# Optimization experiments

Hardware: AMD Instinct MI355X
Metric: run time of the kernel (lower is better)

## Reference

```python
import jax, jax.numpy as jnp
import numpy as np
import math


def _bilinear_sample(fea, gx, gy):
    # fea: (C, Hs, Ws); gx, gy: (P,) pixel coords. zeros padding, align_corners=True.
    C, Hs, Ws = fea.shape
    x0 = jnp.floor(gx)
    y0 = jnp.floor(gy)
    wx = gx - x0
    wy = gy - y0

    def tap(xi, yi):
        valid = (xi >= 0) & (xi <= Ws - 1) & (yi >= 0) & (yi <= Hs - 1)
        xc = jnp.clip(xi, 0, Ws - 1).astype(jnp.int32)
        yc = jnp.clip(yi, 0, Hs - 1).astype(jnp.int32)
        return fea[:, yc, xc] * valid.astype(fea.dtype)  # (C, P)

    return (tap(x0, y0) * (1 - wx) * (1 - wy)
            + tap(x0 + 1, y0) * wx * (1 - wy)
            + tap(x0, y0 + 1) * (1 - wx) * wy
            + tap(x0 + 1, y0 + 1) * wx * wy)


def homo_warping(src_fea, src_proj, ref_proj, depth_values):
    # src_fea: (B,C,Hs,Ws); projs: (B,4,4); depth_values: (B,D,Hr,Wr)
    B, C, Hs, Ws = src_fea.shape
    _, D, Hr, Wr = depth_values.shape
    proj = src_proj @ jnp.linalg.inv(ref_proj)
    rot = proj[:, :3, :3]
    trans = proj[:, :3, 3:4]
    yy, xx = jnp.meshgrid(jnp.arange(Hr, dtype=src_fea.dtype),
                          jnp.arange(Wr, dtype=src_fea.dtype), indexing='ij')
    xyz = jnp.stack([xx.ravel(), yy.ravel(), jnp.ones(Hr * Wr, src_fea.dtype)])  # (3, HW)
    rot_xyz = jnp.einsum('bij,jp->bip', rot, xyz)  # (B,3,HW)
    pts = rot_xyz[:, :, None, :] * depth_values.reshape(B, 1, D, Hr * Wr) + trans[:, :, :, None]
    z = pts[:, 2]
    z = jnp.where(z == 0, 1e-9, z)
    # grid is computed under torch.no_grad() in the original -> stop_gradient
    gx = jax.lax.stop_gradient((pts[:, 0] / z).reshape(B, D * Hr * Wr))
    gy = jax.lax.stop_gradient((pts[:, 1] / z).reshape(B, D * Hr * Wr))
    warped = jax.vmap(_bilinear_sample)(src_fea, gx, gy)  # (B, C, D*Hr*Wr)
    return warped.reshape(B, C, D, Hr, Wr)


def setup_inputs() -> dict:
    key = jax.random.key(0)
    B, C, H, W, D, N = 2, 32, 128, 160, 32, 4
    k1, k2, k3 = jax.random.split(key, 3)
    ref_feature = jax.random.normal(k1, (B, C, H, W), jnp.float32)
    src_features = jax.random.normal(k2, (N, B, C, H, W), jnp.float32)
    # proj_matrices: (B, nviews, 2, 4, 4); [...,0]=extrinsic 4x4, [...,1]=intrinsic 4x4
    K = np.eye(4, dtype=np.float32)
    K[0, 0] = 300.0; K[1, 1] = 300.0; K[0, 2] = W / 2.0; K[1, 2] = H / 2.0
    projs = np.zeros((B, N + 1, 2, 4, 4), np.float32)
    for v in range(N + 1):
        a = 0.03 * v
        Rm = np.array([[np.cos(a), 0.0, np.sin(a)],
                       [0.0, 1.0, 0.0],
                       [-np.sin(a), 0.0, np.cos(a)]], np.float32)
        E = np.eye(4, dtype=np.float32)
        E[:3, :3] = Rm
        E[:3, 3] = np.array([20.0 * v, 5.0 * v, 0.0], np.float32)
        projs[:, v, 0] = E
        projs[:, v, 1] = K
    proj_matrices = jnp.asarray(projs)
    depth_hypo = jnp.broadcast_to(
        jnp.linspace(425.0, 935.0, D, dtype=jnp.float32)[None, :, None, None], (B, D, H, W))
    reg_w = jax.random.normal(k3, (8,), jnp.float32)
    reg_b = jnp.zeros((1,), jnp.float32)
    return {"ref_feature": ref_feature, "src_features": src_features,
            "proj_matrices": proj_matrices, "depth_hypo": depth_hypo,
            "reg_w": reg_w, "reg_b": reg_b}


def reference(ref_feature, src_features, proj_matrices, depth_hypo, reg_w, reg_b):
    attn_temp = 2.0
    G = 8  # group_cor_dim; group_cor=True path
    B, D, H, W = depth_hypo.shape
    C = ref_feature.shape[1]
    ref_proj = proj_matrices[:, 0]
    ref_proj_new = ref_proj[:, 0].at[:, :3, :4].set(
        jnp.einsum('bij,bjk->bik', ref_proj[:, 1, :3, :3], ref_proj[:, 0, :3, :4]))
    # ref_volume broadcast over D via size-1 depth axis (B,G,C/G,1,H,W)
    ref_g = ref_feature.reshape(B, G, C // G, 1, H, W)
    cor_weight_sum = 1e-8
    cor_feats = 0.0
    n_src = src_features.shape[0]
    for src_idx in range(n_src):  # fixed small number of source views
        src_proj = proj_matrices[:, src_idx + 1]
        src_proj_new = src_proj[:, 0].at[:, :3, :4].set(
            jnp.einsum('bij,bjk->bik', src_proj[:, 1, :3, :3], src_proj[:, 0, :3, :4]))
        warped = homo_warping(src_features[src_idx], src_proj_new, ref_proj_new, depth_hypo)
        cor_feat = (warped.reshape(B, G, C // G, D, H, W) * ref_g).mean(2)  # (B,G,D,H,W)
        cor_weight = jax.nn.softmax(cor_feat.sum(1) / attn_temp, axis=1) / math.sqrt(C)  # (B,D,H,W)
        cor_weight_sum = cor_weight_sum + cor_weight
        cor_feats = cor_feats + cor_weight[:, None] * cor_feat
    cor_feats = cor_feats / cor_weight_sum[:, None]
    # regnet stand-in: 1x1x1 conv over the G group channels -> (B,D,H,W) logits
    attn_logits = jnp.einsum('bgdhw,g->bdhw', cor_feats, reg_w) + reg_b[0]
    attn_weight = jax.nn.softmax(attn_logits, axis=1)
    idx = jnp.argmax(attn_weight, axis=1, keepdims=True)
    depth = jnp.take_along_axis(depth_hypo, idx, axis=1).squeeze(1)  # (B,H,W)
    return depth, attn_weight
```

## Files before the change

kernel.cpp:

```cpp
#include <hip/hip_runtime.h>
#include <hip/hip_bf16.h>
#include <math.h>

#define BB 2
#define CC 32
#define HH 128
#define WW 160
#define DD 32
#define NN 4
#define HW (HH * WW)
#define GG 8

typedef float v2f __attribute__((ext_vector_type(2)));

__device__ void compute_mats(int t, const float* __restrict__ proj,
                             float* __restrict__ mats) {
    int b = t >> 2, n = t & 3;
    const float* Er = proj + ((size_t)(b * (NN + 1) + 0) * 2 + 0) * 16;
    const float* Kr = proj + ((size_t)(b * (NN + 1) + 0) * 2 + 1) * 16;
    const float* Es = proj + ((size_t)(b * (NN + 1) + n + 1) * 2 + 0) * 16;
    const float* Ks = proj + ((size_t)(b * (NN + 1) + n + 1) * 2 + 1) * 16;

    double A[4][4], Bm[4][4];
    for (int r = 0; r < 4; r++)
        for (int c = 0; c < 4; c++) {
            if (r < 3) {
                A[r][c]  = (double)Kr[r*4+0]*Er[0*4+c] + (double)Kr[r*4+1]*Er[1*4+c] + (double)Kr[r*4+2]*Er[2*4+c];
                Bm[r][c] = (double)Ks[r*4+0]*Es[0*4+c] + (double)Ks[r*4+1]*Es[1*4+c] + (double)Ks[r*4+2]*Es[2*4+c];
            } else {
                A[r][c]  = (double)Er[12 + c];
                Bm[r][c] = (double)Es[12 + c];
            }
        }
    double M[4][8];
    for (int i = 0; i < 4; i++)
        for (int j = 0; j < 4; j++) { M[i][j] = A[i][j]; M[i][4+j] = (i == j) ? 1.0 : 0.0; }
    for (int col = 0; col < 4; col++) {
        int piv = col;
        for (int r = col + 1; r < 4; r++)
            if (fabs(M[r][col]) > fabs(M[piv][col])) piv = r;
        if (piv != col)
            for (int j = 0; j < 8; j++) { double tmp = M[col][j]; M[col][j] = M[piv][j]; M[piv][j] = tmp; }
        double pv = M[col][col];
        for (int j = 0; j < 8; j++) M[col][j] /= pv;
        for (int r = 0; r < 4; r++) {
            if (r == col) continue;
            double f = M[r][col];
            for (int j = 0; j < 8; j++) M[r][j] -= f * M[col][j];
        }
    }
    float* o = mats + t * 12;
    for (int i = 0; i < 3; i++) {
        double p0 = 0, p1 = 0, p2 = 0, p3 = 0;
        for (int k = 0; k < 4; k++) {
            p0 += Bm[i][k] * M[k][4+0];
            p1 += Bm[i][k] * M[k][4+1];
            p2 += Bm[i][k] * M[k][4+2];
            p3 += Bm[i][k] * M[k][4+3];
        }
        o[i*3+0] = (float)p0; o[i*3+1] = (float)p1; o[i*3+2] = (float)p2;
        o[9 + i] = (float)p3;
    }
}

__global__ __launch_bounds__(256) void prep_transpose(const float* __restrict__ src,
                                                      const float* __restrict__ ref,
                                                      const float* __restrict__ proj,
                                                      float* __restrict__ srcT,
                                                      float* __restrict__ refT,
                                                      float* __restrict__ mats) {
    if (blockIdx.x == 0 && blockIdx.y == 0 && threadIdx.x < 8)
        compute_mats(threadIdx.x, proj, mats);

    __shared__ float t[32][33];
    int slab = blockIdx.y;
    const float* ip;
    float* op;
    if (slab < 8) { ip = src + (size_t)slab * 32 * HW; op = srcT + (size_t)slab * 32 * HW; }
    else          { ip = ref + (size_t)(slab - 8) * 32 * HW; op = refT + (size_t)(slab - 8) * 32 * HW; }
    int hw0 = blockIdx.x * 32;
    int tt = threadIdx.x;
    int c  = tt >> 3;
    int q  = tt & 7;

    float4 rv = *(const float4*)(ip + (size_t)c * HW + hw0 + 4 * q);
    t[c][4 * q + 0] = rv.x;
    t[c][4 * q + 1] = rv.y;
    t[c][4 * q + 2] = rv.z;
    t[c][4 * q + 3] = rv.w;
    __syncthreads();

    int hl = tt >> 3;
    float4 wv;
    wv.x = t[4 * q + 0][hl];
    wv.y = t[4 * q + 1][hl];
    wv.z = t[4 * q + 2][hl];
    wv.w = t[4 * q + 3][hl];
    *(float4*)(op + (size_t)(hw0 + hl) * 32 + 4 * q) = wv;
}

__global__ __launch_bounds__(256) void main_kernel(
    const float* __restrict__ srcT,
    const float* __restrict__ refT,
    const float* __restrict__ depth,
    const float* __restrict__ mats,
    const float* __restrict__ regw,
    const float* __restrict__ regb,
    float* __restrict__ out)
{
    int tid = threadIdx.x;
    int g  = tid & 7;
    int d  = tid >> 3;

    int bid = blockIdx.x;
    int p   = (bid & 7) * ((BB * HW) / 8) + (bid >> 3);
    int b   = p / HW;
    int rem = p - b * HW;
    int y   = rem / WW;
    int x   = rem - y * WW;

    float4 R = *(const float4*)(refT + (size_t)p * 32 + g * 4);
    v2f Rlo = { R.x, R.y }, Rhi = { R.z, R.w };
    float rwg = regw[g];
    float rb  = regb[0];

    __shared__ float4 sW[NN][DD + 1];
    __shared__ int4   sI[NN][DD + 1];
    __shared__ float  sL[NN][DD + 8];
    __shared__ float4 sCWT[DD];
    __shared__ float  sCWS[DD];
    __shared__ float  sE[DD];
    __shared__ float  sDep[DD];

    if (tid < 128) {
        int n0 = tid & 3;
        int dd = tid >> 2;
        float fx = (float)x, fy = (float)y;
        float depM = depth[((size_t)(b * DD + dd) * HH + y) * WW + x];
        const float* Mp = mats + (size_t)(b * NN + n0) * 12;
        float4 m0 = *(const float4*)(Mp);
        float4 m1 = *(const float4*)(Mp + 4);
        float4 m2 = *(const float4*)(Mp + 8);
        float ax = m0.x * fx + m0.y * fy + m0.z;
        float ay = m0.w * fx + m1.x * fy + m1.y;
        float az = m1.z * fx + m1.w * fy + m2.x;
        float px = ax * depM + m2.y;
        float py = ay * depM + m2.z;
        float pz = az * depM + m2.w;
        float z  = (pz == 0.f) ? 1e-9f : pz;
        float rz = __builtin_amdgcn_rcpf(z);
        float gx = px * rz, gy = py * rz;

        float x0f = floorf(gx), y0f = floorf(gy);
        float wx = gx - x0f, wy = gy - y0f;
        bool vx0 = (x0f >= 0.f)  && (x0f <= (float)(WW - 1));
        bool vx1 = (x0f >= -1.f) && (x0f <= (float)(WW - 2));
        bool vy0 = (y0f >= 0.f)  && (y0f <= (float)(HH - 1));
        bool vy1 = (y0f >= -1.f) && (y0f <= (float)(HH - 2));
        float W00 = (vx0 && vy0) ? (1.f - wx) * (1.f - wy) : 0.f;
        float W10 = (vx1 && vy0) ? wx * (1.f - wy)         : 0.f;
        float W01 = (vx0 && vy1) ? (1.f - wx) * wy         : 0.f;
        float W11 = (vx1 && vy1) ? wx * wy                 : 0.f;

        int xi0 = (int)fminf(fmaxf(x0f,       0.f), (float)(WW - 1));
        int xi1 = (int)fminf(fmaxf(x0f + 1.f, 0.f), (float)(WW - 1));
        int yi0 = (int)fminf(fmaxf(y0f,       0.f), (float)(HH - 1));
        int yi1 = (int)fminf(fmaxf(y0f + 1.f, 0.f), (float)(HH - 1));

        sW[n0][dd] = make_float4(W00, W10, W01, W11);
        sI[n0][dd] = make_int4((yi0 * WW + xi0) * 8, (yi0 * WW + xi1) * 8,
                               (yi1 * WW + xi0) * 8, (yi1 * WW + xi1) * 8);
        if (n0 == 0) sDep[dd] = depM;
    }
    __syncthreads();

    float cor[NN];

#pragma unroll
    for (int np = 0; np < 2; np++) {
        int na = 2 * np, nb2 = 2 * np + 1;
        float4 wv0 = sW[na][d];
        int4   iv0 = sI[na][d];
        float4 wv1 = sW[nb2][d];
        int4   iv1 = sI[nb2][d];

        const float4* S0 = (const float4*)(srcT + (size_t)(na  * BB + b) * (32 * HW)) + g;
        const float4* S1 = (const float4*)(srcT + (size_t)(nb2 * BB + b) * (32 * HW)) + g;
        float4 a0 = S0[iv0.x];
        float4 b0 = S0[iv0.y];
        float4 c0 = S0[iv0.z];
        float4 e0 = S0[iv0.w];
        float4 a1 = S1[iv1.x];
        float4 b1 = S1[iv1.y];
        float4 c1 = S1[iv1.z];
        float4 e1 = S1[iv1.w];

        {
            v2f alo = { a0.x, a0.y }, ahi = { a0.z, a0.w };
            v2f blo = { b0.x, b0.y }, bhi = { b0.z, b0.w };
            v2f clo = { c0.x, c0.y }, chi = { c0.z, c0.w };
            v2f elo = { e0.x, e0.y }, ehi = { e0.z, e0.w };
            v2f wlo = wv0.x * alo + wv0.y * blo + wv0.z * clo + wv0.w * elo;
            v2f whi = wv0.x * ahi + wv0.y * bhi + wv0.z * chi + wv0.w * ehi;
            v2f pr  = wlo * Rlo + whi * Rhi;
            float cr = pr.x + pr.y;
            cor[na] = cr;
            float ls = cr;
            ls += __shfl_xor(ls, 1);
            ls += __shfl_xor(ls, 2);
            ls += __shfl_xor(ls, 4);
            if (g == 0) sL[na][d] = ls * 0.125f;
        }
        {
            v2f alo = { a1.x, a1.y }, ahi = { a1.z, a1.w };
            v2f blo = { b1.x, b1.y }, bhi = { b1.z, b1.w };
            v2f clo = { c1.x, c1.y }, chi = { c1.z, c1.w };
            v2f elo = { e1.x, e1.y }, ehi = { e1.z, e1.w };
            v2f wlo = wv1.x * alo + wv1.y * blo + wv1.z * clo + wv1.w * elo;
            v2f whi = wv1.x * ahi + wv1.y * bhi + wv1.z * chi + wv1.w * ehi;
            v2f pr  = wlo * Rlo + whi * Rhi;
            float cr = pr.x + pr.y;
            cor[nb2] = cr;
            float ls = cr;
            ls += __shfl_xor(ls, 1);
            ls += __shfl_xor(ls, 2);
            ls += __shfl_xor(ls, 4);
            if (g == 0) sL[nb2][d] = ls * 0.125f;
        }
    }
    __syncthreads();

    if (tid < 64) {
        int n  = tid >> 4;
        int dh = tid & 15;
        float l0 = sL[n][dh];
        float l1 = sL[n][dh + 16];
        float m = fmaxf(l0, l1);
        m = fmaxf(m, __shfl_xor(m, 1));
        m = fmaxf(m, __shfl_xor(m, 2));
        m = fmaxf(m, __shfl_xor(m, 4));
        m = fmaxf(m, __shfl_xor(m, 8));
        float e0 = __expf(l0 - m), e1 = __expf(l1 - m);
        float s = e0 + e1;
        s += __shfl_xor(s, 1);
        s += __shfl_xor(s, 2);
        s += __shfl_xor(s, 4);
        s += __shfl_xor(s, 8);
        float f = 0.17677669529663687f / s;
        float c0 = e0 * f, c1 = e1 * f;
        ((float*)&sCWT[dh])[n]      = c0 * 0.25f;
        ((float*)&sCWT[dh + 16])[n] = c1 * 0.25f;
        float t0 = c0, t1 = c1;
        t0 += __shfl_xor(t0, 16); t0 += __shfl_xor(t0, 32);
        t1 += __shfl_xor(t1, 16); t1 += __shfl_xor(t1, 32);
        if (n == 0) {
            sCWS[dh]      = t0 + 1e-8f;
            sCWS[dh + 16] = t1 + 1e-8f;
        }
    }
    __syncthreads();

    float4 cwv = sCWT[d];
    float cf = cwv.x * cor[0] + cwv.y * cor[1] + cwv.z * cor[2] + cwv.w * cor[3];
    float v = cf * rwg;
    v += __shfl_xor(v, 1);
    v += __shfl_xor(v, 2);
    v += __shfl_xor(v, 4);
    float logit2 = v * __builtin_amdgcn_rcpf(sCWS[d]) + rb;
    if (g == 0) sE[d] = logit2;
    __syncthreads();

    if (tid < 64) {
        int dl = tid & 31;
        float q = sE[dl];
        float m2 = q;
        m2 = fmaxf(m2, __shfl_xor(m2, 1));
        m2 = fmaxf(m2, __shfl_xor(m2, 2));
        m2 = fmaxf(m2, __shfl_xor(m2, 4));
        m2 = fmaxf(m2, __shfl_xor(m2, 8));
        m2 = fmaxf(m2, __shfl_xor(m2, 16));
        float e2 = __expf(q - m2);
        float t2 = e2;
        t2 += __shfl_xor(t2, 1);
        t2 += __shfl_xor(t2, 2);
        t2 += __shfl_xor(t2, 4);
        t2 += __shfl_xor(t2, 8);
        t2 += __shfl_xor(t2, 16);
        float aw = e2 / t2;
        if (tid < 32)
            out[(size_t)BB * HW + (size_t)(b * DD + dl) * HW + rem] = aw;

        float bv = q; int bi = dl;
#pragma unroll
        for (int s = 1; s <= 16; s <<= 1) {
            float ov = __shfl_xor(bv, s);
            int   oi = __shfl_xor(bi, s);
            if (ov > bv || (ov == bv && oi < bi)) { bv = ov; bi = oi; }
        }
        if (tid < 32 && dl == bi) out[p] = sDep[bi];
    }
}

extern "C" void kernel_launch(void* const* d_in, const int* in_sizes, int n_in,
                              void* d_out, int out_size, void* d_ws, size_t ws_size,
                              hipStream_t stream) {
    const float* ref   = (const float*)d_in[0];
    const float* src   = (const float*)d_in[1];
    const float* proj  = (const float*)d_in[2];
    const float* depth = (const float*)d_in[3];
    const float* regw  = (const float*)d_in[4];
    const float* regb  = (const float*)d_in[5];
    float* out = (float*)d_out;

    float* ws   = (float*)d_ws;
    float* mats = ws;
    float* srcT = ws + 256;
    float* refT = srcT + (size_t)NN * BB * HW * 32;

    prep_transpose<<<dim3(HW / 32, 10), 256, 0, stream>>>(src, ref, proj,
                                                          srcT, refT, mats);
    main_kernel<<<BB * HW, 256, 0, stream>>>(srcT, refT, depth, mats,
                                             regw, regb, out);
}
```

Baseline: 184.4 us.

## Issue all source-view gathers upfront and drop shared-memory transpose in prep

The main kernel now issues all 16 bilinear tap loads for the four source views before the blends and interleaves the shuffle reductions, so more memory requests are in flight per thread. The per-view partial sums go to shared memory in one packed float4 store per depth. Tap offsets are precomputed as byte offsets to simplify address arithmetic. The prep transpose drops the LDS staging and barrier: each thread does strided scalar reads and writes float4 rows, with four tiles per block, trading coalesced reads for fewer syncs and blocks. This raises register pressure in the main kernel.

New measurement: 190.9 us. 1.04x slower.

```diff
diff --git a/kernel.cpp b/kernel.cpp
--- a/kernel.cpp
+++ b/kernel.cpp
@@ -1,5 +1,4 @@
 #include <hip/hip_runtime.h>
-#include <hip/hip_bf16.h>
 #include <math.h>
 
 #define BB 2
@@ -72,31 +71,39 @@
     if (blockIdx.x == 0 && blockIdx.y == 0 && threadIdx.x < 8)
         compute_mats(threadIdx.x, proj, mats);
 
-    __shared__ float t[32][33];
     int slab = blockIdx.y;
     const float* ip;
     float* op;
     if (slab < 8) { ip = src + (size_t)slab * 32 * HW; op = srcT + (size_t)slab * 32 * HW; }
     else          { ip = ref + (size_t)(slab - 8) * 32 * HW; op = refT + (size_t)(slab - 8) * 32 * HW; }
-    int hw0 = blockIdx.x * 32;
+
     int tt = threadIdx.x;
-    int c  = tt >> 3;
     int q  = tt & 7;
-
-    float4 rv = *(const float4*)(ip + (size_t)c * HW + hw0 + 4 * q);
-    t[c][4 * q + 0] = rv.x;
-    t[c][4 * q + 1] = rv.y;
-    t[c][4 * q + 2] = rv.z;
-    t[c][4 * q + 3] = rv.w;
-    __syncthreads();
-
     int hl = tt >> 3;
-    float4 wv;
-    wv.x = t[4 * q + 0][hl];
-    wv.y = t[4 * q + 1][hl];
-    wv.z = t[4 * q + 2][hl];
-    wv.w = t[4 * q + 3][hl];
-    *(float4*)(op + (size_t)(hw0 + hl) * 32 + 4 * q) = wv;
+    int c0 = 4 * q;
+    int hwb = blockIdx.x * 128 + hl;
+#pragma unroll
+    for (int t4 = 0; t4 < 4; t4++) {
+        int hw = hwb + t4 * 32;
+        float va = ip[(size_t)(c0 + 0) * HW + hw];
+        float vb = ip[(size_t)(c0 + 1) * HW + hw];
+        float vc = ip[(size_t)(c0 + 2) * HW + hw];
+        float vd = ip[(size_t)(c0 + 3) * HW + hw];
+        *(float4*)(op + (size_t)hw * 32 + c0) = make_float4(va, vb, vc, vd);
+    }
+}
+
+__device__ __forceinline__ float blend_dot(float4 wv, float4 A, float4 Bv,
+                                           float4 Cv, float4 Ev,
+                                           v2f Rlo, v2f Rhi) {
+    v2f alo = { A.x,  A.y  }, ahi = { A.z,  A.w  };
+    v2f blo = { Bv.x, Bv.y }, bhi = { Bv.z, Bv.w };
+    v2f clo = { Cv.x, Cv.y }, chi = { Cv.z, Cv.w };
+    v2f elo = { Ev.x, Ev.y }, ehi = { Ev.z, Ev.w };
+    v2f wlo = wv.x * alo + wv.y * blo + wv.z * clo + wv.w * elo;
+    v2f whi = wv.x * ahi + wv.y * bhi + wv.z * chi + wv.w * ehi;
+    v2f pr  = wlo * Rlo + whi * Rhi;
+    return pr.x + pr.y;
 }
 
 __global__ __launch_bounds__(256) void main_kernel(
@@ -126,7 +133,7 @@
 
     __shared__ float4 sW[NN][DD + 1];
     __shared__ int4   sI[NN][DD + 1];
-    __shared__ float  sL[NN][DD + 8];
+    __shared__ __align__(16) float sLp[DD][8];
     __shared__ float4 sCWT[DD];
     __shared__ float  sCWS[DD];
     __shared__ float  sE[DD];
@@ -168,89 +175,81 @@
         int yi1 = (int)fminf(fmaxf(y0f + 1.f, 0.f), (float)(HH - 1));
 
         sW[n0][dd] = make_float4(W00, W10, W01, W11);
-        sI[n0][dd] = make_int4((yi0 * WW + xi0) * 8, (yi0 * WW + xi1) * 8,
-                               (yi1 * WW + xi0) * 8, (yi1 * WW + xi1) * 8);
+        sI[n0][dd] = make_int4((yi0 * WW + xi0) * 128, (yi0 * WW + xi1) * 128,
+                               (yi1 * WW + xi0) * 128, (yi1 * WW + xi1) * 128);
         if (n0 == 0) sDep[dd] = depM;
     }
     __syncthreads();
 
-    float cor[NN];
-
-#pragma unroll
-    for (int np = 0; np < 2; np++) {
-        int na = 2 * np, nb2 = 2 * np + 1;
-        float4 wv0 = sW[na][d];
-        int4   iv0 = sI[na][d];
-        float4 wv1 = sW[nb2][d];
-        int4   iv1 = sI[nb2][d];
-
-        const float4* S0 = (const float4*)(srcT + (size_t)(na  * BB + b) * (32 * HW)) + g;
-        const float4* S1 = (const float4*)(srcT + (size_t)(nb2 * BB + b) * (32 * HW)) + g;
-        float4 a0 = S0[iv0.x];
-        float4 b0 = S0[iv0.y];
-        float4 c0 = S0[iv0.z];
-        float4 e0 = S0[iv0.w];
-        float4 a1 = S1[iv1.x];
-        float4 b1 = S1[iv1.y];
-        float4 c1 = S1[iv1.z];
-        float4 e1 = S1[iv1.w];
-
-        {
-            v2f alo = { a0.x, a0.y }, ahi = { a0.z, a0.w };
-            v2f blo = { b0.x, b0.y }, bhi = { b0.z, b0.w };
-            v2f clo = { c0.x, c0.y }, chi = { c0.z, c0.w };
-            v2f elo = { e0.x, e0.y }, ehi = { e0.z, e0.w };
-            v2f wlo = wv0.x * alo + wv0.y * blo + wv0.z * clo + wv0.w * elo;
-            v2f whi = wv0.x * ahi + wv0.y * bhi + wv0.z * chi + wv0.w * ehi;
-            v2f pr  = wlo * Rlo + whi * Rhi;
-            float cr = pr.x + pr.y;
-            cor[na] = cr;
-            float ls = cr;
-            ls += __shfl_xor(ls, 1);
-            ls += __shfl_xor(ls, 2);
-            ls += __shfl_xor(ls, 4);
-            if (g == 0) sL[na][d] = ls * 0.125f;
-        }
-        {
-            v2f alo = { a1.x, a1.y }, ahi = { a1.z, a1.w };
-            v2f blo = { b1.x, b1.y }, bhi = { b1.z, b1.w };
-            v2f clo = { c1.x, c1.y }, chi = { c1.z, c1.w };
-            v2f elo = { e1.x, e1.y }, ehi = { e1.z, e1.w };
-            v2f wlo = wv1.x * alo + wv1.y * blo + wv1.z * clo + wv1.w * elo;
-            v2f whi = wv1.x * ahi + wv1.y * bhi + wv1.z * chi + wv1.w * ehi;
-            v2f pr  = wlo * Rlo + whi * Rhi;
-            float cr = pr.x + pr.y;
-            cor[nb2] = cr;
-            float ls = cr;
-            ls += __shfl_xor(ls, 1);
-            ls += __shfl_xor(ls, 2);
-            ls += __shfl_xor(ls, 4);
-            if (g == 0) sL[nb2][d] = ls * 0.125f;
-        }
-    }
+    float4 wv0 = sW[0][d], wv1 = sW[1][d], wv2 = sW[2][d], wv3 = sW[3][d];
+    int4   iv0 = sI[0][d], iv1 = sI[1][d], iv2 = sI[2][d], iv3 = sI[3][d];
+    unsigned g16 = (unsigned)(g * 16);
+
+    const char* S0 = (const char*)srcT + (size_t)(0 * BB + b) * (32 * HW) * 4;
+    const char* S1 = (const char*)srcT + (size_t)(1 * BB + b) * (32 * HW) * 4;
+    const char* S2 = (const char*)srcT + (size_t)(2 * BB + b) * (32 * HW) * 4;
+    const char* S3 = (const char*)srcT + (size_t)(3 * BB + b) * (32 * HW) * 4;
+
+    float4 a0 = *(const float4*)(S0 + ((unsigned)iv0.x + g16));
+    float4 b0 = *(const float4*)(S0 + ((unsigned)iv0.y + g16));
+    float4 c0 = *(const float4*)(S0 + ((unsigned)iv0.z + g16));
+    float4 e0 = *(const float4*)(S0 + ((unsigned)iv0.w + g16));
+    float4 a1 = *(const float4*)(S1 + ((unsigned)iv1.x + g16));
+    float4 b1 = *(const float4*)(S1 + ((unsigned)iv1.y + g16));
+    float4 c1 = *(const float4*)(S1 + ((unsigned)iv1.z + g16));
+    float4 e1 = *(const float4*)(S1 + ((unsigned)iv1.w + g16));
+    float4 a2 = *(const float4*)(S2 + ((unsigned)iv2.x + g16));
+    float4 b2 = *(const float4*)(S2 + ((unsigned)iv2.y + g16));
+    float4 c2 = *(const float4*)(S2 + ((unsigned)iv2.z + g16));
+    float4 e2 = *(const float4*)(S2 + ((unsigned)iv2.w + g16));
+
+    float cor0 = blend_dot(wv0, a0, b0, c0, e0, Rlo, Rhi);
+
+    float4 a3 = *(const float4*)(S3 + ((unsigned)iv3.x + g16));
+    float4 b3 = *(const float4*)(S3 + ((unsigned)iv3.y + g16));
+    float4 c3 = *(const float4*)(S3 + ((unsigned)iv3.z + g16));
+    float4 e3 = *(const float4*)(S3 + ((unsigned)iv3.w + g16));
+
+    float cor1 = blend_dot(wv1, a1, b1, c1, e1, Rlo, Rhi);
+    float cor2 = blend_dot(wv2, a2, b2, c2, e2, Rlo, Rhi);
+
+    float r0 = cor0, r1 = cor1, r2 = cor2;
+    r0 += __shfl_xor(r0, 1); r1 += __shfl_xor(r1, 1); r2 += __shfl_xor(r2, 1);
+    r0 += __shfl_xor(r0, 2); r1 += __shfl_xor(r1, 2); r2 += __shfl_xor(r2, 2);
+    r0 += __shfl_xor(r0, 4); r1 += __shfl_xor(r1, 4); r2 += __shfl_xor(r2, 4);
+
+    float cor3 = blend_dot(wv3, a3, b3, c3, e3, Rlo, Rhi);
+    float r3 = cor3;
+    r3 += __shfl_xor(r3, 1);
+    r3 += __shfl_xor(r3, 2);
+    r3 += __shfl_xor(r3, 4);
+
+    if (g == 0)
+        *(float4*)&sLp[d][0] = make_float4(r0 * 0.125f, r1 * 0.125f,
+                                           r2 * 0.125f, r3 * 0.125f);
     __syncthreads();
 
     if (tid < 64) {
         int n  = tid >> 4;
         int dh = tid & 15;
-        float l0 = sL[n][dh];
-        float l1 = sL[n][dh + 16];
+        float l0 = sLp[dh][n];
+        float l1 = sLp[dh + 16][n];
         float m = fmaxf(l0, l1);
         m = fmaxf(m, __shfl_xor(m, 1));
         m = fmaxf(m, __shfl_xor(m, 2));
         m = fmaxf(m, __shfl_xor(m, 4));
         m = fmaxf(m, __shfl_xor(m, 8));
-        float e0 = __expf(l0 - m), e1 = __expf(l1 - m);
-        float s = e0 + e1;
+        float e0s = __expf(l0 - m), e1s = __expf(l1 - m);
+        float s = e0s + e1s;
         s += __shfl_xor(s, 1);
         s += __shfl_xor(s, 2);
         s += __shfl_xor(s, 4);
         s += __shfl_xor(s, 8);
         float f = 0.17677669529663687f / s;
-        float c0 = e0 * f, c1 = e1 * f;
-        ((float*)&sCWT[dh])[n]      = c0 * 0.25f;
-        ((float*)&sCWT[dh + 16])[n] = c1 * 0.25f;
-        float t0 = c0, t1 = c1;
+        float c0s = e0s * f, c1s = e1s * f;
+        ((float*)&sCWT[dh])[n]      = c0s * 0.25f;
+        ((float*)&sCWT[dh + 16])[n] = c1s * 0.25f;
+        float t0 = c0s, t1 = c1s;
         t0 += __shfl_xor(t0, 16); t0 += __shfl_xor(t0, 32);
         t1 += __shfl_xor(t1, 16); t1 += __shfl_xor(t1, 32);
         if (n == 0) {
@@ -261,7 +260,7 @@
     __syncthreads();
 
     float4 cwv = sCWT[d];
-    float cf = cwv.x * cor[0] + cwv.y * cor[1] + cwv.z * cor[2] + cwv.w * cor[3];
+    float cf = cwv.x * cor0 + cwv.y * cor1 + cwv.z * cor2 + cwv.w * cor3;
     float v = cf * rwg;
     v += __shfl_xor(v, 1);
     v += __shfl_xor(v, 2);
@@ -317,8 +316,8 @@
     float* srcT = ws + 256;
     float* refT = srcT + (size_t)NN * BB * HW * 32;
 
-    prep_transpose<<<dim3(HW / 32, 10), 256, 0, stream>>>(src, ref, proj,
-                                                          srcT, refT, mats);
+    prep_transpose<<<dim3(HW / 128, 10), 256, 0, stream>>>(src, ref, proj,
+                                                           srcT, refT, mats);
     main_kernel<<<BB * HW, 256, 0, stream>>>(srcT, refT, depth, mats,
                                              regw, regb, out);
 }
```

## Process two pixels per block and overlap softmax stages across pixels

Applied to the files above, without the earlier changes.

Each block now handles two adjacent pixels instead of one, halving the grid size. The homography setup for both pixels runs across all 256 threads at once. The per-pixel softmax statistics and final argmax phases are interleaved with the gather and compute of the other pixel, so the partial-wave serial phases overlap with useful work. This cuts block launch overhead and idle threads, at the cost of doubled shared memory and register pressure per block.

New measurement: 188.9 us. 1.02x slower.

```diff
diff --git a/kernel.cpp b/kernel.cpp
--- a/kernel.cpp
+++ b/kernel.cpp
@@ -1,5 +1,4 @@
 #include <hip/hip_runtime.h>
-#include <hip/hip_bf16.h>
 #include <math.h>
 
 #define BB 2
@@ -99,6 +98,131 @@
     *(float4*)(op + (size_t)(hw0 + hl) * 32 + 4 * q) = wv;
 }
 
+__device__ __forceinline__ void homog_setup(int t, int bb, int y, int x,
+        const float* __restrict__ depth, const float* __restrict__ mats,
+        float4 (*sWs)[DD + 1], int4 (*sIs)[DD + 1], float* sDeps) {
+    int n0 = t & 3;
+    int dd = t >> 2;
+    float fx = (float)x, fy = (float)y;
+    float depM = depth[((size_t)(bb * DD + dd) * HH + y) * WW + x];
+    const float* Mp = mats + (size_t)(bb * NN + n0) * 12;
+    float4 m0 = *(const float4*)(Mp);
+    float4 m1 = *(const float4*)(Mp + 4);
+    float4 m2 = *(const float4*)(Mp + 8);
+    float ax = m0.x * fx + m0.y * fy + m0.z;
+    float ay = m0.w * fx + m1.x * fy + m1.y;
+    float az = m1.z * fx + m1.w * fy + m2.x;
+    float px = ax * depM + m2.y;
+    float py = ay * depM + m2.z;
+    float pz = az * depM + m2.w;
+    float z  = (pz == 0.f) ? 1e-9f : pz;
+    float rz = __builtin_amdgcn_rcpf(z);
+    float gx = px * rz, gy = py * rz;
+
+    float x0f = floorf(gx), y0f = floorf(gy);
+    float wx = gx - x0f, wy = gy - y0f;
+    bool vx0 = (x0f >= 0.f)  && (x0f <= (float)(WW - 1));
+    bool vx1 = (x0f >= -1.f) && (x0f <= (float)(WW - 2));
+    bool vy0 = (y0f >= 0.f)  && (y0f <= (float)(HH - 1));
+    bool vy1 = (y0f >= -1.f) && (y0f <= (float)(HH - 2));
+    float W00 = (vx0 && vy0) ? (1.f - wx) * (1.f - wy) : 0.f;
+    float W10 = (vx1 && vy0) ? wx * (1.f - wy)         : 0.f;
+    float W01 = (vx0 && vy1) ? (1.f - wx) * wy         : 0.f;
+    float W11 = (vx1 && vy1) ? wx * wy                 : 0.f;
+
+    int xi0 = (int)fminf(fmaxf(x0f,       0.f), (float)(WW - 1));
+    int xi1 = (int)fminf(fmaxf(x0f + 1.f, 0.f), (float)(WW - 1));
+    int yi0 = (int)fminf(fmaxf(y0f,       0.f), (float)(HH - 1));
+    int yi1 = (int)fminf(fmaxf(y0f + 1.f, 0.f), (float)(HH - 1));
+
+    sWs[n0][dd] = make_float4(W00, W10, W01, W11);
+    sIs[n0][dd] = make_int4((yi0 * WW + xi0) * 8, (yi0 * WW + xi1) * 8,
+                            (yi1 * WW + xi0) * 8, (yi1 * WW + xi1) * 8);
+    if (n0 == 0) sDeps[dd] = depM;
+}
+
+__device__ __forceinline__ float consume_src(float4 wv, float4 A, float4 Bv,
+                                             float4 Cv, float4 Ev,
+                                             v2f Rlo, v2f Rhi, int g, int d,
+                                             float* sLrow) {
+    v2f alo = { A.x,  A.y  }, ahi = { A.z,  A.w  };
+    v2f blo = { Bv.x, Bv.y }, bhi = { Bv.z, Bv.w };
+    v2f clo = { Cv.x, Cv.y }, chi = { Cv.z, Cv.w };
+    v2f elo = { Ev.x, Ev.y }, ehi = { Ev.z, Ev.w };
+    v2f wlo = wv.x * alo + wv.y * blo + wv.z * clo + wv.w * elo;
+    v2f whi = wv.x * ahi + wv.y * bhi + wv.z * chi + wv.w * ehi;
+    v2f pr  = wlo * Rlo + whi * Rhi;
+    float cr = pr.x + pr.y;
+    float ls = cr;
+    ls += __shfl_xor(ls, 1);
+    ls += __shfl_xor(ls, 2);
+    ls += __shfl_xor(ls, 4);
+    if (g == 0) sLrow[d] = ls * 0.125f;
+    return cr;
+}
+
+__device__ __forceinline__ void stats_fn(int lane, const float (*sLs)[DD + 8],
+                                         float4* sCWTs, float* sCWSs) {
+    int n  = lane >> 4;
+    int dh = lane & 15;
+    float l0 = sLs[n][dh];
+    float l1 = sLs[n][dh + 16];
+    float m = fmaxf(l0, l1);
+    m = fmaxf(m, __shfl_xor(m, 1));
+    m = fmaxf(m, __shfl_xor(m, 2));
+    m = fmaxf(m, __shfl_xor(m, 4));
+    m = fmaxf(m, __shfl_xor(m, 8));
+    float e0s = __expf(l0 - m), e1s = __expf(l1 - m);
+    float s = e0s + e1s;
+    s += __shfl_xor(s, 1);
+    s += __shfl_xor(s, 2);
+    s += __shfl_xor(s, 4);
+    s += __shfl_xor(s, 8);
+    float f = 0.17677669529663687f / s;
+    float c0s = e0s * f, c1s = e1s * f;
+    ((float*)&sCWTs[dh])[n]      = c0s * 0.25f;
+    ((float*)&sCWTs[dh + 16])[n] = c1s * 0.25f;
+    float t0 = c0s, t1 = c1s;
+    t0 += __shfl_xor(t0, 16); t0 += __shfl_xor(t0, 32);
+    t1 += __shfl_xor(t1, 16); t1 += __shfl_xor(t1, 32);
+    if (n == 0) {
+        sCWSs[dh]      = t0 + 1e-8f;
+        sCWSs[dh + 16] = t1 + 1e-8f;
+    }
+}
+
+__device__ __forceinline__ void final_fn(int lane, const float* sEs,
+                                         const float* sDeps, float* out,
+                                         int b, int rem, int p) {
+    int dl = lane & 31;
+    float q = sEs[dl];
+    float m2 = q;
+    m2 = fmaxf(m2, __shfl_xor(m2, 1));
+    m2 = fmaxf(m2, __shfl_xor(m2, 2));
+    m2 = fmaxf(m2, __shfl_xor(m2, 4));
+    m2 = fmaxf(m2, __shfl_xor(m2, 8));
+    m2 = fmaxf(m2, __shfl_xor(m2, 16));
+    float e2 = __expf(q - m2);
+    float t2 = e2;
+    t2 += __shfl_xor(t2, 1);
+    t2 += __shfl_xor(t2, 2);
+    t2 += __shfl_xor(t2, 4);
+    t2 += __shfl_xor(t2, 8);
+    t2 += __shfl_xor(t2, 16);
+    float aw = e2 / t2;
+    if (lane < 32)
+        out[(size_t)BB * HW + (size_t)(b * DD + dl) * HW + rem] = aw;
+
+    float bv = q; int bi = dl;
+#pragma unroll
+    for (int s = 1; s <= 16; s <<= 1) {
+        float ov = __shfl_xor(bv, s);
+        int   oi = __shfl_xor(bi, s);
+        if (ov > bv || (ov == bv && oi < bi)) { bv = ov; bi = oi; }
+    }
+    if (lane < 32 && dl == bi) out[p] = sDeps[bi];
+}
+
 __global__ __launch_bounds__(256) void main_kernel(
     const float* __restrict__ srcT,
     const float* __restrict__ refT,
@@ -112,193 +236,106 @@
     int g  = tid & 7;
     int d  = tid >> 3;
 
-    int bid = blockIdx.x;
-    int p   = (bid & 7) * ((BB * HW) / 8) + (bid >> 3);
-    int b   = p / HW;
-    int rem = p - b * HW;
-    int y   = rem / WW;
-    int x   = rem - y * WW;
-
-    float4 R = *(const float4*)(refT + (size_t)p * 32 + g * 4);
-    v2f Rlo = { R.x, R.y }, Rhi = { R.z, R.w };
+    int q   = blockIdx.x;
+    int w   = (q & 7) * ((BB * HW / 2) / 8) + (q >> 3);
+    int p0  = 2 * w;
+    int p1  = p0 + 1;
+    int b   = p0 / HW;
+    int rem0 = p0 - b * HW;
+    int rem1 = rem0 + 1;
+    int y0p = rem0 / WW, x0p = rem0 - y0p * WW;
+    int y1p = rem1 / WW, x1p = rem1 - y1p * WW;
+
+    float4 RA = *(const float4*)(refT + (size_t)p0 * 32 + g * 4);
+    float4 RB = *(const float4*)(refT + (size_t)p1 * 32 + g * 4);
+    v2f RAlo = { RA.x, RA.y }, RAhi = { RA.z, RA.w };
+    v2f RBlo = { RB.x, RB.y }, RBhi = { RB.z, RB.w };
     float rwg = regw[g];
     float rb  = regb[0];
 
-    __shared__ float4 sW[NN][DD + 1];
-    __shared__ int4   sI[NN][DD + 1];
-    __shared__ float  sL[NN][DD + 8];
-    __shared__ float4 sCWT[DD];
-    __shared__ float  sCWS[DD];
-    __shared__ float  sE[DD];
-    __shared__ float  sDep[DD];
-
-    if (tid < 128) {
-        int n0 = tid & 3;
-        int dd = tid >> 2;
-        float fx = (float)x, fy = (float)y;
-        float depM = depth[((size_t)(b * DD + dd) * HH + y) * WW + x];
-        const float* Mp = mats + (size_t)(b * NN + n0) * 12;
-        float4 m0 = *(const float4*)(Mp);
-        float4 m1 = *(const float4*)(Mp + 4);
-        float4 m2 = *(const float4*)(Mp + 8);
-        float ax = m0.x * fx + m0.y * fy + m0.z;
-        float ay = m0.w * fx + m1.x * fy + m1.y;
-        float az = m1.z * fx + m1.w * fy + m2.x;
-        float px = ax * depM + m2.y;
-        float py = ay * depM + m2.z;
-        float pz = az * depM + m2.w;
-        float z  = (pz == 0.f) ? 1e-9f : pz;
-        float rz = __builtin_amdgcn_rcpf(z);
-        float gx = px * rz, gy = py * rz;
-
-        float x0f = floorf(gx), y0f = floorf(gy);
-        float wx = gx - x0f, wy = gy - y0f;
-        bool vx0 = (x0f >= 0.f)  && (x0f <= (float)(WW - 1));
-        bool vx1 = (x0f >= -1.f) && (x0f <= (float)(WW - 2));
-        bool vy0 = (y0f >= 0.f)  && (y0f <= (float)(HH - 1));
-        bool vy1 = (y0f >= -1.f) && (y0f <= (float)(HH - 2));
-        float W00 = (vx0 && vy0) ? (1.f - wx) * (1.f - wy) : 0.f;
-        float W10 = (vx1 && vy0) ? wx * (1.f - wy)         : 0.f;
-        float W01 = (vx0 && vy1) ? (1.f - wx) * wy         : 0.f;
-        float W11 = (vx1 && vy1) ? wx * wy                 : 0.f;
-
-        int xi0 = (int)fminf(fmaxf(x0f,       0.f), (float)(WW - 1));
-        int xi1 = (int)fminf(fmaxf(x0f + 1.f, 0.f), (float)(WW - 1));
-        int yi0 = (int)fminf(fmaxf(y0f,       0.f), (float)(HH - 1));
-        int yi1 = (int)fminf(fmaxf(y0f + 1.f, 0.f), (float)(HH - 1));
-
-        sW[n0][dd] = make_float4(W00, W10, W01, W11);
-        sI[n0][dd] = make_int4((yi0 * WW + xi0) * 8, (yi0 * WW + xi1) * 8,
-                               (yi1 * WW + xi0) * 8, (yi1 * WW + xi1) * 8);
-        if (n0 == 0) sDep[dd] = depM;
-    }
-    __syncthreads();
-
-    float cor[NN];
-
-#pragma unroll
-    for (int np = 0; np < 2; np++) {
-        int na = 2 * np, nb2 = 2 * np + 1;
-        float4 wv0 = sW[na][d];
-        int4   iv0 = sI[na][d];
-        float4 wv1 = sW[nb2][d];
-        int4   iv1 = sI[nb2][d];
-
-        const float4* S0 = (const float4*)(srcT + (size_t)(na  * BB + b) * (32 * HW)) + g;
-        const float4* S1 = (const float4*)(srcT + (size_t)(nb2 * BB + b) * (32 * HW)) + g;
-        float4 a0 = S0[iv0.x];
-        float4 b0 = S0[iv0.y];
-        float4 c0 = S0[iv0.z];
-        float4 e0 = S0[iv0.w];
-        float4 a1 = S1[iv1.x];
-        float4 b1 = S1[iv1.y];
-        float4 c1 = S1[iv1.z];
-        float4 e1 = S1[iv1.w];
-
-        {
-            v2f alo = { a0.x, a0.y }, ahi = { a0.z, a0.w };
-            v2f blo = { b0.x, b0.y }, bhi = { b0.z, b0.w };
-            v2f clo = { c0.x, c0.y }, chi = { c0.z, c0.w };
-            v2f elo = { e0.x, e0.y }, ehi = { e0.z, e0.w };
-            v2f wlo = wv0.x * alo + wv0.y * blo + wv0.z * clo + wv0.w * elo;
-            v2f whi = wv0.x * ahi + wv0.y * bhi + wv0.z * chi + wv0.w * ehi;
-            v2f pr  = wlo * Rlo + whi * Rhi;
-            float cr = pr.x + pr.y;
-            cor[na] = cr;
-            float ls = cr;
-            ls += __shfl_xor(ls, 1);
-            ls += __shfl_xor(ls, 2);
-            ls += __shfl_xor(ls, 4);
-            if (g == 0) sL[na][d] = ls * 0.125f;
-        }
-        {
-            v2f alo = { a1.x, a1.y }, ahi = { a1.z, a1.w };
-            v2f blo = { b1.x, b1.y }, bhi = { b1.z, b1.w };
-            v2f clo = { c1.x, c1.y }, chi = { c1.z, c1.w };
-            v2f elo = { e1.x, e1.y }, ehi = { e1.z, e1.w };
-            v2f wlo = wv1.x * alo + wv1.y * blo + wv1.z * clo + wv1.w * elo;
-            v2f whi = wv1.x * ahi + wv1.y * bhi + wv1.z * chi + wv1.w * ehi;
-            v2f pr  = wlo * Rlo + whi * Rhi;
-            float cr = pr.x + pr.y;
-            cor[nb2] = cr;
-            float ls = cr;
-            ls += __shfl_xor(ls, 1);
-            ls += __shfl_xor(ls, 2);
-            ls += __shfl_xor(ls, 4);
-            if (g == 0) sL[nb2][d] = ls * 0.125f;
-        }
-    }
-    __syncthreads();
-
-    if (tid < 64) {
-        int n  = tid >> 4;
-        int dh = tid & 15;
-        float l0 = sL[n][dh];
-        float l1 = sL[n][dh + 16];
-        float m = fmaxf(l0, l1);
-        m = fmaxf(m, __shfl_xor(m, 1));
-        m = fmaxf(m, __shfl_xor(m, 2));
-        m = fmaxf(m, __shfl_xor(m, 4));
-        m = fmaxf(m, __shfl_xor(m, 8));
-        float e0 = __expf(l0 - m), e1 = __expf(l1 - m);
-        float s = e0 + e1;
-        s += __shfl_xor(s, 1);
-        s += __shfl_xor(s, 2);
-        s += __shfl_xor(s, 4);
-        s += __shfl_xor(s, 8);
-        float f = 0.17677669529663687f / s;
-        float c0 = e0 * f, c1 = e1 * f;
-        ((float*)&sCWT[dh])[n]      = c0 * 0.25f;
-        ((float*)&sCWT[dh + 16])[n] = c1 * 0.25f;
-        float t0 = c0, t1 = c1;
-        t0 += __shfl_xor(t0, 16); t0 += __shfl_xor(t0, 32);
-        t1 += __shfl_xor(t1, 16); t1 += __shfl_xor(t1, 32);
-        if (n == 0) {
-            sCWS[dh]      = t0 + 1e-8f;
-            sCWS[dh + 16] = t1 + 1e-8f;
-        }
-    }
-    __syncthreads();
-
-    float4 cwv = sCWT[d];
-    float cf = cwv.x * cor[0] + cwv.y * cor[1] + cwv.z * cor[2] + cwv.w * cor[3];
-    float v = cf * rwg;
-    v += __shfl_xor(v, 1);
-    v += __shfl_xor(v, 2);
-    v += __shfl_xor(v, 4);
-    float logit2 = v * __builtin_amdgcn_rcpf(sCWS[d]) + rb;
-    if (g == 0) sE[d] = logit2;
-    __syncthreads();
-
-    if (tid < 64) {
-        int dl = tid & 31;
-        float q = sE[dl];
-        float m2 = q;
-        m2 = fmaxf(m2, __shfl_xor(m2, 1));
-        m2 = fmaxf(m2, __shfl_xor(m2, 2));
-        m2 = fmaxf(m2, __shfl_xor(m2, 4));
-        m2 = fmaxf(m2, __shfl_xor(m2, 8));
-        m2 = fmaxf(m2, __shfl_xor(m2, 16));
-        float e2 = __expf(q - m2);
-        float t2 = e2;
-        t2 += __shfl_xor(t2, 1);
-        t2 += __shfl_xor(t2, 2);
-        t2 += __shfl_xor(t2, 4);
-        t2 += __shfl_xor(t2, 8);
-        t2 += __shfl_xor(t2, 16);
-        float aw = e2 / t2;
-        if (tid < 32)
-            out[(size_t)BB * HW + (size_t)(b * DD + dl) * HW + rem] = aw;
-
-        float bv = q; int bi = dl;
-#pragma unroll
-        for (int s = 1; s <= 16; s <<= 1) {
-            float ov = __shfl_xor(bv, s);
-            int   oi = __shfl_xor(bi, s);
-            if (ov > bv || (ov == bv && oi < bi)) { bv = ov; bi = oi; }
-        }
-        if (tid < 32 && dl == bi) out[p] = sDep[bi];
-    }
+    __shared__ float4 sW[2][NN][DD + 1];
+    __shared__ int4   sI[2][NN][DD + 1];
+    __shared__ float  sL[2][NN][DD + 8];
+    __shared__ float4 sCWT[2][DD];
+    __shared__ float  sCWS[2][DD];
+    __shared__ float  sE[2][DD];
+    __shared__ float  sDep[2][DD];
+
+    if (tid < 128) homog_setup(tid,       b, y0p, x0p, depth, mats, sW[0], sI[0], sDep[0]);
+    else           homog_setup(tid - 128, b, y1p, x1p, depth, mats, sW[1], sI[1], sDep[1]);
+    __syncthreads();
+
+    const float4* S0 = (const float4*)(srcT + (size_t)(0 * BB + b) * (32 * HW)) + g;
+    const float4* S1 = (const float4*)(srcT + (size_t)(1 * BB + b) * (32 * HW)) + g;
+    const float4* S2 = (const float4*)(srcT + (size_t)(2 * BB + b) * (32 * HW)) + g;
+    const float4* S3 = (const float4*)(srcT + (size_t)(3 * BB + b) * (32 * HW)) + g;
+
+    float corA[NN], corB[NN];
+
+    {
+        float4 wv0 = sW[0][0][d]; int4 iv0 = sI[0][0][d];
+        float4 wv1 = sW[0][1][d]; int4 iv1 = sI[0][1][d];
+        float4 a0 = S0[iv0.x], b0 = S0[iv0.y], c0 = S0[iv0.z], e0 = S0[iv0.w];
+        float4 a1 = S1[iv1.x], b1 = S1[iv1.y], c1 = S1[iv1.z], e1 = S1[iv1.w];
+        corA[0] = consume_src(wv0, a0, b0, c0, e0, RAlo, RAhi, g, d, &sL[0][0][0]);
+        corA[1] = consume_src(wv1, a1, b1, c1, e1, RAlo, RAhi, g, d, &sL[0][1][0]);
+
+        float4 wv2 = sW[0][2][d]; int4 iv2 = sI[0][2][d];
+        float4 wv3 = sW[0][3][d]; int4 iv3 = sI[0][3][d];
+        float4 a2 = S2[iv2.x], b2 = S2[iv2.y], c2 = S2[iv2.z], e2 = S2[iv2.w];
+        float4 a3 = S3[iv3.x], b3 = S3[iv3.y], c3 = S3[iv3.z], e3 = S3[iv3.w];
+        corA[2] = consume_src(wv2, a2, b2, c2, e2, RAlo, RAhi, g, d, &sL[0][2][0]);
+        corA[3] = consume_src(wv3, a3, b3, c3, e3, RAlo, RAhi, g, d, &sL[0][3][0]);
+    }
+    __syncthreads();
+
+    {
+        float4 wv0 = sW[1][0][d]; int4 iv0 = sI[1][0][d];
+        float4 wv1 = sW[1][1][d]; int4 iv1 = sI[1][1][d];
+        float4 a0 = S0[iv0.x], b0 = S0[iv0.y], c0 = S0[iv0.z], e0 = S0[iv0.w];
+        float4 a1 = S1[iv1.x], b1 = S1[iv1.y], c1 = S1[iv1.z], e1 = S1[iv1.w];
+
+        if (tid < 64) stats_fn(tid, sL[0], sCWT[0], sCWS[0]);
+
+        corB[0] = consume_src(wv0, a0, b0, c0, e0, RBlo, RBhi, g, d, &sL[1][0][0]);
+        corB[1] = consume_src(wv1, a1, b1, c1, e1, RBlo, RBhi, g, d, &sL[1][1][0]);
+
+        float4 wv2 = sW[1][2][d]; int4 iv2 = sI[1][2][d];
+        float4 wv3 = sW[1][3][d]; int4 iv3 = sI[1][3][d];
+        float4 a2 = S2[iv2.x], b2 = S2[iv2.y], c2 = S2[iv2.z], e2 = S2[iv2.w];
+        float4 a3 = S3[iv3.x], b3 = S3[iv3.y], c3 = S3[iv3.z], e3 = S3[iv3.w];
+        corB[2] = consume_src(wv2, a2, b2, c2, e2, RBlo, RBhi, g, d, &sL[1][2][0]);
+        corB[3] = consume_src(wv3, a3, b3, c3, e3, RBlo, RBhi, g, d, &sL[1][3][0]);
+    }
+    __syncthreads();
+
+    {
+        float4 cwv = sCWT[0][d];
+        float cf = cwv.x * corA[0] + cwv.y * corA[1] + cwv.z * corA[2] + cwv.w * corA[3];
+        float vv = cf * rwg;
+        vv += __shfl_xor(vv, 1);
+        vv += __shfl_xor(vv, 2);
+        vv += __shfl_xor(vv, 4);
+        float logit2 = vv * __builtin_amdgcn_rcpf(sCWS[0][d]) + rb;
+        if (g == 0) sE[0][d] = logit2;
+    }
+    if (tid >= 64 && tid < 128) stats_fn(tid - 64, sL[1], sCWT[1], sCWS[1]);
+    __syncthreads();
+
+    {
+        float4 cwv = sCWT[1][d];
+        float cf = cwv.x * corB[0] + cwv.y * corB[1] + cwv.z * corB[2] + cwv.w * corB[3];
+        float vv = cf * rwg;
+        vv += __shfl_xor(vv, 1);
+        vv += __shfl_xor(vv, 2);
+        vv += __shfl_xor(vv, 4);
+        float logit2 = vv * __builtin_amdgcn_rcpf(sCWS[1][d]) + rb;
+        if (g == 0) sE[1][d] = logit2;
+    }
+    if (tid < 64) final_fn(tid, sE[0], sDep[0], out, b, rem0, p0);
+    __syncthreads();
+
+    if (tid < 64) final_fn(tid, sE[1], sDep[1], out, b, rem1, p1);
 }
 
 extern "C" void kernel_launch(void* const* d_in, const int* in_sizes, int n_in,
@@ -319,6 +356,6 @@
 
     prep_transpose<<<dim3(HW / 32, 10), 256, 0, stream>>>(src, ref, proj,
                                                           srcT, refT, mats);
-    main_kernel<<<BB * HW, 256, 0, stream>>>(srcT, refT, depth, mats,
-                                             regw, regb, out);
-}
+    main_kernel<<<BB * HW / 2, 256, 0, stream>>>(srcT, refT, depth, mats,
+                                                 regw, regb, out);
+}
```
